# Optimization experiments

Measured on AMD Instinct MI355X. Metric: run time of the kernel, lower is better.

Reference implementation:

```python
import jax, jax.numpy as jnp
import numpy as np
import math

N_HEADS = 16
D_EFF = 64
ROPE_BASE = 500.0


def _rope(x, cos, sin):
    # x: (b, h, L, d_eff); cos/sin: (L, d_eff//2)
    x_even = x[..., 0::2]
    x_odd = x[..., 1::2]
    rot = jnp.stack([x_even * cos - x_odd * sin,
                     x_even * sin + x_odd * cos], axis=-1)
    return rot.reshape(x.shape)


def setup_inputs() -> dict:
    key = jax.random.key(0)
    ks = jax.random.split(key, 5)
    B, L, D = 1, 2048, 1024
    X = jax.random.normal(ks[0], (B, L, D), dtype=jnp.float32)
    # causal mask (1 = keep, 0 = masked), broadcastable to (B, h, L, L)
    mask = jnp.tril(jnp.ones((L, L), dtype=jnp.int32))[None, :, :]
    s = 1.0 / math.sqrt(D)
    Wq = jax.random.normal(ks[1], (D, D), dtype=jnp.float32) * s
    Wk = jax.random.normal(ks[2], (D, D), dtype=jnp.float32) * s
    Wv = jax.random.normal(ks[3], (D, D), dtype=jnp.float32) * s
    Wo = jax.random.normal(ks[4], (D, D), dtype=jnp.float32) * s
    return {"X": X, "mask": mask, "Wq": Wq, "Wk": Wk, "Wv": Wv, "Wo": Wo}


def reference(X, mask, Wq, Wk, Wv, Wo):
    b, L, d_model = X.shape
    h, d = N_HEADS, D_EFF
    d_full = h * d

    def split_heads(Y):
        return Y.reshape(b, L, h, d).transpose(0, 2, 1, 3)  # (b,h,L,d)

    Q = split_heads(X @ Wq)
    K = split_heads(X @ Wk)
    V = split_heads(X @ Wv)

    # interleaved RoPE, base 500
    inv_freq = 1.0 / (ROPE_BASE ** (jnp.arange(0, d, 2, dtype=jnp.float32) / d))
    freqs = jnp.arange(L, dtype=jnp.float32)[:, None] * inv_freq  # (L, d/2)
    cos, sin = jnp.cos(freqs), jnp.sin(freqs)
    Q = _rope(Q, cos, sin)
    K = _rope(K, cos, sin)

    S = jnp.einsum('bhqd,bhkd->bhqk', Q, K) / math.sqrt(d)
    S = jnp.where(mask[:, None, :, :] == 0, jnp.float32(-1e9), S)
    # NOTE: faithful to original torch code: softmax over the HEADS axis (dim=1)
    A = jax.nn.softmax(S, axis=1)
    Y = jnp.einsum('bhqk,bhkd->bhqd', A, V)
    Y = Y.transpose(0, 2, 1, 3).reshape(b, L, d_full)
    Y = Y @ Wo
    return Y * math.sqrt(d_model / d_full)
```

## Files before the change

kernel.cpp:

```cpp
#include <hip/hip_runtime.h>
#include <stdint.h>
#include <stddef.h>
#include <math.h>

typedef __attribute__((ext_vector_type(8))) short bf16x8;
typedef __attribute__((ext_vector_type(4))) short short4v;
typedef __attribute__((ext_vector_type(4))) float f32x4;

__device__ __forceinline__ short f2bf(float f) {
  union { float f; uint32_t u; } x; x.f = f;
  return (short)((x.u + 0x7fffu + ((x.u >> 16) & 1u)) >> 16);
}
__device__ __forceinline__ float bf2f(short s) {
  union { uint32_t u; float f; } x; x.u = ((uint32_t)(uint16_t)s) << 16;
  return x.f;
}
__device__ __forceinline__ uint32_t cvt_pk_bf16(float a, float b) {
  uint32_t r;
  asm("v_cvt_pk_bf16_f32 %0, %1, %2" : "=v"(r) : "v"(a), "v"(b));
  return r;
}

__device__ __forceinline__ void gload_lds16(const void* g, void* lds) {
  __builtin_amdgcn_global_load_lds(
      (const __attribute__((address_space(1))) void*)g,
      (__attribute__((address_space(3))) void*)lds, 16, 0, 0);
}

__global__ __launch_bounds__(256) void cast_b(const float* __restrict__ s,
                                              short* __restrict__ d) {
  int i4 = (blockIdx.x * 256 + threadIdx.x) * 4;
  float4 v = *(const float4*)&s[i4];
  short4v r = { f2bf(v.x), f2bf(v.y), f2bf(v.z), f2bf(v.w) };
  *(short4v*)&d[i4] = r;
}

__global__ __launch_bounds__(256) void reduce_y(const short* __restrict__ Ypc,
                                                const float* __restrict__ Cvs,
                                                short* __restrict__ o) {
  int q = blockIdx.x;
  int j = q >> 5, qr = q & 31;
  int col = threadIdx.x * 4;
  float a0 = Cvs[col + 0], a1 = Cvs[col + 1], a2 = Cvs[col + 2], a3 = Cvs[col + 3];
  int cf = (j - 2) >> 2;
  for (int c = 0; c <= cf; c++) {
    int slot = (c <= 7) ? (c + 8 * (j - 4 * c - 2)) : ((15 - c) + 8 * j);
    const short* p = Ypc + ((size_t)slot * 32 + qr) * 1024 + col;
    short4v v = *(const short4v*)p;
    a0 += bf2f(v[0]); a1 += bf2f(v[1]); a2 += bf2f(v[2]); a3 += bf2f(v[3]);
  }
  if ((j & 3) < 2) {
    int cp = j >> 2;
    int slot = (cp <= 7) ? (cp + 8 * (64 + (j & 3)))
                         : ((15 - cp) + 8 * (66 + (j & 3)));
    const short* p = Ypc + ((size_t)slot * 32 + qr) * 1024 + col;
    short4v v = *(const short4v*)p;
    a0 += bf2f(v[0]); a1 += bf2f(v[1]); a2 += bf2f(v[2]); a3 += bf2f(v[3]);
  }
  uint32_t u0 = cvt_pk_bf16(a0, a1), u1 = cvt_pk_bf16(a2, a3);
  short4v rr = { (short)u0, (short)(u0 >> 16), (short)u1, (short)(u1 >> 16) };
  *(short4v*)&o[(size_t)q * 1024 + col] = rr;
}

__global__ __launch_bounds__(256) void transW(const float* __restrict__ Wq,
                                              const float* __restrict__ Wk,
                                              const float* __restrict__ Wv,
                                              const float* __restrict__ Wo,
                                              short* __restrict__ WcatT,
                                              short* __restrict__ WoT) {
  int z = blockIdx.z;
  const float* src = (z == 0) ? Wq : (z == 1) ? Wk : (z == 2) ? Wv : Wo;
  short* dst = (z == 3) ? WoT : WcatT + (size_t)z * 1024 * 1024;
  __shared__ float tl[32][33];
  int tx = threadIdx.x & 31, ty = threadIdx.x >> 5;
  int kk0 = blockIdx.x * 32;
  int nn0 = blockIdx.y * 32;
#pragma unroll
  for (int j = 0; j < 4; j++)
    tl[ty + j * 8][tx] = src[(size_t)(kk0 + ty + j * 8) * 1024 + nn0 + tx];
  __syncthreads();
#pragma unroll
  for (int j = 0; j < 4; j++)
    dst[(size_t)(nn0 + ty + j * 8) * 1024 + kk0 + tx] = f2bf(tl[tx][ty + j * 8]);
}

__global__ __launch_bounds__(256) void transpose_v(const short* __restrict__ Vb,
                                                   short* __restrict__ Vt) {
  __shared__ short tv[64][72];
  int h = blockIdx.y, k0 = blockIdx.x * 64;
  int tid = threadIdx.x;
#pragma unroll
  for (int j = 0; j < 2; j++) {
    int idx = tid + j * 256;
    int row = idx >> 3, c = idx & 7;
    bf16x8 v = *(const bf16x8*)&Vb[((size_t)h * 2048 + k0 + row) * 64 + c * 8];
#pragma unroll
    for (int t = 0; t < 8; t++) tv[row][c * 8 + t] = v[t];
  }
  __syncthreads();
#pragma unroll
  for (int j = 0; j < 2; j++) {
    int idx = tid + j * 256;
    int d = idx >> 3, c = idx & 7;
    bf16x8 v;
#pragma unroll
    for (int t = 0; t < 8; t++) v[t] = tv[c * 8 + t][d];
    *(bf16x8*)&Vt[((size_t)h * 64 + d) * 2048 + k0 + c * 8] = v;
  }
}

__global__ __launch_bounds__(256) void vsum(const short* __restrict__ Vb,
                                            float* __restrict__ Cvs) {
  __shared__ float red[16][17];
  int h = blockIdx.x >> 2, dq = blockIdx.x & 3;
  int dl = threadIdx.x & 15, ks = threadIdx.x >> 4;
  int d = dq * 16 + dl;
  float acc = 0.f;
  const short* base = &Vb[((size_t)h * 2048 + ks * 128) * 64 + d];
#pragma unroll 8
  for (int k = 0; k < 128; k++) acc += bf2f(base[(size_t)k * 64]);
  red[dl][ks] = acc;
  __syncthreads();
  if (threadIdx.x < 16) {
    float sum = 0.f;
#pragma unroll
    for (int i = 0; i < 16; i++) sum += red[threadIdx.x][i];
    Cvs[h * 64 + dq * 16 + threadIdx.x] = sum * 0.0625f;
  }
}

template <int MODE>
__global__ __launch_bounds__(256, 4)
void gemm_kernel(const short* __restrict__ A, const short* __restrict__ B,
                 int N, int K, float* __restrict__ C,
                 short* __restrict__ Qb, short* __restrict__ Kb,
                 short* __restrict__ Vb) {
  __shared__ __attribute__((aligned(16))) short lga[128 * 64];
  __shared__ __attribute__((aligned(16))) short lgb[128 * 64];
  const int tid = threadIdx.x;
  const int lane = tid & 63;
  const int w = tid >> 6;
  const int l15 = lane & 15;
  const int quad = lane >> 4;
  const int wm = w >> 1, wn = w & 1;
  const int m0 = blockIdx.x * 128, n0 = blockIdx.y * 128;
  const int rsub = lane >> 3;
  const int cpos = lane & 7;

  f32x4 acc[4][4];
#pragma unroll
  for (int i = 0; i < 4; i++)
#pragma unroll
    for (int j = 0; j < 4; j++) acc[i][j] = (f32x4){0.f, 0.f, 0.f, 0.f};

  for (int kb = 0; kb < K; kb += 64) {
    __syncthreads();
#pragma unroll
    for (int j = 0; j < 4; j++) {
      int r = (w * 4 + j) * 8 + rsub;
      int kc = cpos ^ rsub;
      gload_lds16(A + (size_t)(m0 + r) * K + kb + kc * 8, &lga[(w * 4 + j) * 512]);
      gload_lds16(B + (size_t)(n0 + r) * K + kb + kc * 8, &lgb[(w * 4 + j) * 512]);
    }
    __syncthreads();
#pragma unroll
    for (int kk = 0; kk < 2; kk++) {
      bf16x8 af[4], bfr[4];
#pragma unroll
      for (int t = 0; t < 4; t++) {
        int row = wm * 64 + t * 16 + l15;
        int pc = (kk * 4 + quad) ^ (row & 7);
        af[t] = *(const bf16x8*)&lga[row * 64 + pc * 8];
        int rowb = wn * 64 + t * 16 + l15;
        int pcb = (kk * 4 + quad) ^ (rowb & 7);
        bfr[t] = *(const bf16x8*)&lgb[rowb * 64 + pcb * 8];
      }
#pragma unroll
      for (int mt = 0; mt < 4; mt++)
#pragma unroll
        for (int nt = 0; nt < 4; nt++)
          acc[mt][nt] = __builtin_amdgcn_mfma_f32_16x16x32_bf16(
              af[mt], bfr[nt], acc[mt][nt], 0, 0, 0);
    }
  }

  if (MODE == 0) {
#pragma unroll
    for (int mt = 0; mt < 4; mt++) {
      int q = m0 + wm * 64 + mt * 16 + quad * 4;
#pragma unroll
      for (int nt = 0; nt < 4; nt++) {
        int n = n0 + wn * 64 + nt * 16 + l15;
#pragma unroll
        for (int r = 0; r < 4; r++) C[(size_t)(q + r) * N + n] = acc[mt][nt][r];
      }
    }
  } else {
#pragma unroll
    for (int mt = 0; mt < 4; mt++) {
#pragma unroll
      for (int nt = 0; nt < 4; nt++) {
        int n = n0 + wn * 64 + nt * 16 + l15;
        int mat = n >> 10;
        int h = (n >> 6) & 15;
        int d = n & 63;
#pragma unroll
        for (int r = 0; r < 4; r++) {
          int q = m0 + wm * 64 + mt * 16 + quad * 4 + r;
          float v = acc[mt][nt][r];
          float o = __shfl_xor(v, 1, 64);
          if (mat < 2) {
            int i = d >> 1;
            float ang = (float)q * __builtin_exp2f(-(float)i * 0.2801807588956902f);
            float sn, cs;
            __sincosf(ang, &sn, &cs);
            float rv = (d & 1) ? (o * sn + v * cs) : (v * cs - o * sn);
            short* dst = (mat == 0) ? Qb : Kb;
            dst[((size_t)h * 2048 + q) * 64 + d] = f2bf(rv);
          } else {
            Vb[((size_t)h * 2048 + q) * 64 + d] = f2bf(v);
          }
        }
      }
    }
  }
}

__global__ __launch_bounds__(1024, 2)
void attn_kernel(const short* __restrict__ Qb, const short* __restrict__ Kb,
                 const short* __restrict__ Vt, short* __restrict__ Ypc) {
  __shared__ short Sb[16 * 32 * 72];
  const int tid = threadIdx.x;
  const int lane = tid & 63;
  const int h = tid >> 6;
  const int l15 = lane & 15, quad = lane >> 4;
  const int b = blockIdx.x;
  const int x = b & 7, s = b >> 3;
  int c, j, ng;
  const int n1 = 62 - 4 * x;
  if (s < n1)      { c = x;      j = 4 * x + 2 + s;        ng = 2; }
  else if (s < 64) { c = 15 - x; j = s;                    ng = 2; }
  else if (s < 66) { c = x;      j = 4 * x + (s - 64);     ng = 1; }
  else             { c = 15 - x; j = 60 - 4 * x + (s - 66); ng = 1; }
  const int q0 = j * 32;
  const int g0 = 2 * c;

  bf16x8 qf[2][2];
#pragma unroll
  for (int qs = 0; qs < 2; qs++)
#pragma unroll
    for (int cc = 0; cc < 2; cc++)
      qf[qs][cc] = *(const bf16x8*)&Qb[((size_t)h * 2048 + q0 + qs * 16 + l15) * 64 +
                                       cc * 32 + quad * 8];

  f32x4 yacc[2][4];
#pragma unroll
  for (int i = 0; i < 2; i++)
#pragma unroll
    for (int jj = 0; jj < 4; jj++) yacc[i][jj] = (f32x4){0.f, 0.f, 0.f, 0.f};

  for (int gi = 0; gi < ng; gi++) {
    const int k0 = (g0 + gi) * 64;
#pragma unroll
    for (int st = 0; st < 4; st++) {
      const short* kb = &Kb[((size_t)h * 2048 + k0 + st * 16 + l15) * 64 + quad * 8];
      bf16x8 kf0 = *(const bf16x8*)kb;
      bf16x8 kf1 = *(const bf16x8*)(kb + 32);
#pragma unroll
      for (int qs = 0; qs < 2; qs++) {
        f32x4 sa = (f32x4){0.f, 0.f, 0.f, 0.f};
        sa = __builtin_amdgcn_mfma_f32_16x16x32_bf16(qf[qs][0], kf0, sa, 0, 0, 0);
        sa = __builtin_amdgcn_mfma_f32_16x16x32_bf16(qf[qs][1], kf1, sa, 0, 0, 0);
        const float cs = 0.18033688011112042f;
        uint32_t u0 = cvt_pk_bf16(sa[0] * cs, sa[1] * cs);
        uint32_t u1 = cvt_pk_bf16(sa[2] * cs, sa[3] * cs);
        int rb = (h * 32 + qs * 16 + quad * 4) * 72 + st * 16 + l15;
        Sb[rb]       = (short)u0;
        Sb[rb + 72]  = (short)(u0 >> 16);
        Sb[rb + 144] = (short)u1;
        Sb[rb + 216] = (short)(u1 >> 16);
      }
    }
    __syncthreads();
#pragma unroll
    for (int pp = 0; pp < 2; pp++) {
      int p = tid + pp * 1024;
      int q = p >> 6, kl = p & 63;
      int base = q * 72 + kl;
      float t[16];
      float sum = 0.f;
#pragma unroll
      for (int hh = 0; hh < 16; hh++) {
        float e = __builtin_exp2f(bf2f(Sb[hh * 2304 + base]));
        t[hh] = e;
        sum += e;
      }
      bool msk = (k0 + kl) > (q0 + q);
      float rs = msk ? 0.f : 1.f / sum;
      float offv = msk ? 0.f : 0.0625f;
#pragma unroll
      for (int hh = 0; hh < 16; hh += 2) {
        uint32_t u = cvt_pk_bf16(t[hh] * rs - offv, t[hh + 1] * rs - offv);
        Sb[hh * 2304 + base]       = (short)u;
        Sb[(hh + 1) * 2304 + base] = (short)(u >> 16);
      }
    }
    __syncthreads();
#pragma unroll
    for (int kk = 0; kk < 2; kk++) {
      bf16x8 af0 = *(const bf16x8*)&Sb[(h * 32 + l15) * 72 + kk * 32 + quad * 8];
      bf16x8 af1 = *(const bf16x8*)&Sb[(h * 32 + 16 + l15) * 72 + kk * 32 + quad * 8];
#pragma unroll
      for (int nt = 0; nt < 4; nt++) {
        bf16x8 vf = *(const bf16x8*)&Vt[((size_t)h * 64 + nt * 16 + l15) * 2048 +
                                        k0 + kk * 32 + quad * 8];
        yacc[0][nt] = __builtin_amdgcn_mfma_f32_16x16x32_bf16(af0, vf, yacc[0][nt],
                                                              0, 0, 0);
        yacc[1][nt] = __builtin_amdgcn_mfma_f32_16x16x32_bf16(af1, vf, yacc[1][nt],
                                                              0, 0, 0);
      }
    }
    __syncthreads();
  }
  short* Y = Ypc + (size_t)b * 32 * 1024;
#pragma unroll
  for (int qs = 0; qs < 2; qs++) {
#pragma unroll
    for (int nt = 0; nt < 4; nt++) {
      int col = h * 64 + nt * 16 + l15;
#pragma unroll
      for (int rr = 0; rr < 4; rr++)
        Y[(size_t)(qs * 16 + quad * 4 + rr) * 1024 + col] = f2bf(yacc[qs][nt][rr]);
    }
  }
}

extern "C" void kernel_launch(void* const* d_in, const int* in_sizes, int n_in,
                              void* d_out, int out_size, void* d_ws, size_t ws_size,
                              hipStream_t stream) {
  (void)in_sizes; (void)n_in; (void)out_size; (void)ws_size;
  const float* X  = (const float*)d_in[0];
  const float* Wq = (const float*)d_in[2];
  const float* Wk = (const float*)d_in[3];
  const float* Wv = (const float*)d_in[4];
  const float* Wo = (const float*)d_in[5];
  char* ws = (char*)d_ws;
  const size_t MB = 1024 * 1024;
  short* Xbf   = (short*)(ws + 0);
  short* WcatT = (short*)(ws + 4 * MB);
  short* WoT   = (short*)(ws + 10 * MB);
  short* Qb    = (short*)(ws + 12 * MB);
  short* Kb    = (short*)(ws + 16 * MB);
  short* Vb    = (short*)(ws + 20 * MB);
  short* Vt    = (short*)(ws + 24 * MB);
  short* Ypc   = (short*)(ws + 28 * MB);
  float* Cvs   = (float*)(ws + 63 * MB);
  short* Ycbf  = Xbf;
  float* out   = (float*)d_out;

  cast_b<<<dim3(2048), dim3(256), 0, stream>>>(X, Xbf);
  transW<<<dim3(32, 32, 4), dim3(256), 0, stream>>>(Wq, Wk, Wv, Wo, WcatT, WoT);
  gemm_kernel<1><<<dim3(16, 24), dim3(256), 0, stream>>>(Xbf, WcatT, 3072, 1024,
                                                         nullptr, Qb, Kb, Vb);
  transpose_v<<<dim3(32, 16), dim3(256), 0, stream>>>(Vb, Vt);
  vsum<<<dim3(64), dim3(256), 0, stream>>>(Vb, Cvs);
  attn_kernel<<<dim3(544), dim3(1024), 0, stream>>>(Qb, Kb, Vt, Ypc);
  reduce_y<<<dim3(2048), dim3(256), 0, stream>>>(Ypc, Cvs, Ycbf);
  gemm_kernel<0><<<dim3(16, 8), dim3(256), 0, stream>>>(Ycbf, WoT, 1024, 1024,
                                                        out, nullptr, nullptr, nullptr);
}
```

Before: 212.6 us.

## Fuse V column-sum into transpose, add smaller-tile output GEMM, relax QKV occupancy

Drops the separate vsum kernel. The per-head V column sums are now computed inside transpose_v from its shared tile and accumulated with atomicAdd into Cvs, which cast_b zeroes at the start. A dedicated output-projection GEMM with 128x64 tiles launches 256 blocks instead of 128, to fill more CUs. The QKV GEMM launch bound goes from 4 to 2 waves per SIMD, which gives it more registers. The cost is float atomics with a nondeterministic summation order, and possibly lower occupancy in the QKV GEMM.

```diff
diff --git a/kernel.cpp b/kernel.cpp
--- a/kernel.cpp
+++ b/kernel.cpp
@@ -28,7 +28,12 @@
 }
 
 __global__ __launch_bounds__(256) void cast_b(const float* __restrict__ s,
-                                              short* __restrict__ d) {
+                                              short* __restrict__ d,
+                                              float* __restrict__ Cvs) {
+  if (blockIdx.x == 0) {
+    int c4 = threadIdx.x * 4;
+    Cvs[c4] = 0.f; Cvs[c4 + 1] = 0.f; Cvs[c4 + 2] = 0.f; Cvs[c4 + 3] = 0.f;
+  }
   int i4 = (blockIdx.x * 256 + threadIdx.x) * 4;
   float4 v = *(const float4*)&s[i4];
   short4v r = { f2bf(v.x), f2bf(v.y), f2bf(v.z), f2bf(v.w) };
@@ -85,7 +90,8 @@
 }
 
 __global__ __launch_bounds__(256) void transpose_v(const short* __restrict__ Vb,
-                                                   short* __restrict__ Vt) {
+                                                   short* __restrict__ Vt,
+                                                   float* __restrict__ Cvs) {
   __shared__ short tv[64][72];
   int h = blockIdx.y, k0 = blockIdx.x * 64;
   int tid = threadIdx.x;
@@ -107,30 +113,16 @@
     for (int t = 0; t < 8; t++) v[t] = tv[c * 8 + t][d];
     *(bf16x8*)&Vt[((size_t)h * 64 + d) * 2048 + k0 + c * 8] = v;
   }
-}
-
-__global__ __launch_bounds__(256) void vsum(const short* __restrict__ Vb,
-                                            float* __restrict__ Cvs) {
-  __shared__ float red[16][17];
-  int h = blockIdx.x >> 2, dq = blockIdx.x & 3;
-  int dl = threadIdx.x & 15, ks = threadIdx.x >> 4;
-  int d = dq * 16 + dl;
-  float acc = 0.f;
-  const short* base = &Vb[((size_t)h * 2048 + ks * 128) * 64 + d];
+  if (tid < 64) {
+    float s = 0.f;
 #pragma unroll 8
-  for (int k = 0; k < 128; k++) acc += bf2f(base[(size_t)k * 64]);
-  red[dl][ks] = acc;
-  __syncthreads();
-  if (threadIdx.x < 16) {
-    float sum = 0.f;
-#pragma unroll
-    for (int i = 0; i < 16; i++) sum += red[threadIdx.x][i];
-    Cvs[h * 64 + dq * 16 + threadIdx.x] = sum * 0.0625f;
+    for (int k = 0; k < 64; k++) s += bf2f(tv[k][tid]);
+    atomicAdd(&Cvs[h * 64 + tid], s * 0.0625f);
   }
 }
 
 template <int MODE>
-__global__ __launch_bounds__(256, 4)
+__global__ __launch_bounds__(256, 2)
 void gemm_kernel(const short* __restrict__ A, const short* __restrict__ B,
                  int N, int K, float* __restrict__ C,
                  short* __restrict__ Qb, short* __restrict__ Kb,
@@ -222,6 +214,76 @@
           }
         }
       }
+    }
+  }
+}
+
+__global__ __launch_bounds__(256, 4)
+void gemm_o(const short* __restrict__ A, const short* __restrict__ B,
+            float* __restrict__ C) {
+  __shared__ __attribute__((aligned(16))) short lga[128 * 64];
+  __shared__ __attribute__((aligned(16))) short lgb[64 * 64];
+  const int tid = threadIdx.x;
+  const int lane = tid & 63;
+  const int w = tid >> 6;
+  const int l15 = lane & 15;
+  const int quad = lane >> 4;
+  const int m0 = blockIdx.x * 128, n0 = blockIdx.y * 64;
+  const int rsub = lane >> 3;
+  const int cpos = lane & 7;
+
+  f32x4 acc[2][4];
+#pragma unroll
+  for (int i = 0; i < 2; i++)
+#pragma unroll
+    for (int j = 0; j < 4; j++) acc[i][j] = (f32x4){0.f, 0.f, 0.f, 0.f};
+
+  for (int kb = 0; kb < 1024; kb += 64) {
+    __syncthreads();
+    int kc = cpos ^ rsub;
+#pragma unroll
+    for (int j = 0; j < 4; j++) {
+      int r = (w * 4 + j) * 8 + rsub;
+      gload_lds16(A + (size_t)(m0 + r) * 1024 + kb + kc * 8, &lga[(w * 4 + j) * 512]);
+    }
+#pragma unroll
+    for (int j = 0; j < 2; j++) {
+      int r = (w * 2 + j) * 8 + rsub;
+      gload_lds16(B + (size_t)(n0 + r) * 1024 + kb + kc * 8, &lgb[(w * 2 + j) * 512]);
+    }
+    __syncthreads();
+#pragma unroll
+    for (int kk = 0; kk < 2; kk++) {
+      bf16x8 af[2], bfr[4];
+#pragma unroll
+      for (int t = 0; t < 2; t++) {
+        int row = w * 32 + t * 16 + l15;
+        int pc = (kk * 4 + quad) ^ (row & 7);
+        af[t] = *(const bf16x8*)&lga[row * 64 + pc * 8];
+      }
+#pragma unroll
+      for (int t = 0; t < 4; t++) {
+        int rowb = t * 16 + l15;
+        int pcb = (kk * 4 + quad) ^ (rowb & 7);
+        bfr[t] = *(const bf16x8*)&lgb[rowb * 64 + pcb * 8];
+      }
+#pragma unroll
+      for (int mt = 0; mt < 2; mt++)
+#pragma unroll
+        for (int nt = 0; nt < 4; nt++)
+          acc[mt][nt] = __builtin_amdgcn_mfma_f32_16x16x32_bf16(
+              af[mt], bfr[nt], acc[mt][nt], 0, 0, 0);
+    }
+  }
+
+#pragma unroll
+  for (int mt = 0; mt < 2; mt++) {
+    int q = m0 + w * 32 + mt * 16 + quad * 4;
+#pragma unroll
+    for (int nt = 0; nt < 4; nt++) {
+      int n = n0 + nt * 16 + l15;
+#pragma unroll
+      for (int r = 0; r < 4; r++) C[(size_t)(q + r) * 1024 + n] = acc[mt][nt][r];
     }
   }
 }
@@ -358,14 +420,12 @@
   short* Ycbf  = Xbf;
   float* out   = (float*)d_out;
 
-  cast_b<<<dim3(2048), dim3(256), 0, stream>>>(X, Xbf);
+  cast_b<<<dim3(2048), dim3(256), 0, stream>>>(X, Xbf, Cvs);
   transW<<<dim3(32, 32, 4), dim3(256), 0, stream>>>(Wq, Wk, Wv, Wo, WcatT, WoT);
   gemm_kernel<1><<<dim3(16, 24), dim3(256), 0, stream>>>(Xbf, WcatT, 3072, 1024,
                                                          nullptr, Qb, Kb, Vb);
-  transpose_v<<<dim3(32, 16), dim3(256), 0, stream>>>(Vb, Vt);
-  vsum<<<dim3(64), dim3(256), 0, stream>>>(Vb, Cvs);
+  transpose_v<<<dim3(32, 16), dim3(256), 0, stream>>>(Vb, Vt, Cvs);
   attn_kernel<<<dim3(544), dim3(1024), 0, stream>>>(Qb, Kb, Vt, Ypc);
   reduce_y<<<dim3(2048), dim3(256), 0, stream>>>(Ypc, Cvs, Ycbf);
-  gemm_kernel<0><<<dim3(16, 8), dim3(256), 0, stream>>>(Ycbf, WoT, 1024, 1024,
-                                                        out, nullptr, nullptr, nullptr);
-}
+  gemm_o<<<dim3(16, 16), dim3(256), 0, stream>>>(Ycbf, WoT, out);
+}
```

After: 203.6 us. 4.2% less time.
